# Kernel optimization log

Hardware: AMD Instinct MI355X
Metric: run time of the kernel (lower is better)

Reference implementation:

```python
import jax, jax.numpy as jnp
import numpy as np

NUM_HEADS = 6
DIM = 192
WS = (2, 6, 12)          # window size (z, h, w)
DATA = (8, 96, 180)      # padded (plev, lat, lon)
SHIFT = (1, 3, 6)


def _position_index(ws):
    Z, H, W = ws
    zi, zj = np.arange(Z), -np.arange(Z) * Z
    hi, hj = np.arange(H), -np.arange(H) * H
    w = np.arange(W)
    c1 = np.stack(np.meshgrid(zi, hi, w, indexing='ij')).reshape(3, -1)
    c2 = np.stack(np.meshgrid(zj, hj, w, indexing='ij')).reshape(3, -1)
    coords = (c1[:, :, None] - c2[:, None, :]).transpose(1, 2, 0).copy()
    coords[:, :, 2] += W - 1
    coords[:, :, 1] *= 2 * W - 1
    coords[:, :, 0] *= (2 * W - 1) * H * H
    return coords.sum(-1).reshape(-1).astype(np.int32)


def _shift_mask(data, ws, ss):
    Z, H, W = data
    img = np.zeros((Z, H, W))
    cnt = 0
    for z in ((0, -ss[0]), (-ss[0], None)):
        for h in ((0, -ss[1]), (-ss[1], None)):
            for w in ((0, None),):  # lam=False: longitude is cyclic, no w split
                img[z[0]:z[1], h[0]:h[1], w[0]:w[1]] = cnt
                cnt += 1
    m = img.reshape(Z // ws[0], ws[0], H // ws[1], ws[1], W // ws[2], ws[2])
    m = m.transpose(0, 2, 4, 1, 3, 5).reshape(-1, ws[0] * ws[1] * ws[2])
    diff = m[:, None, :] - m[:, :, None]
    return np.where(diff != 0, -100.0, 0.0).astype(np.float32)


def setup_inputs() -> dict:
    key = jax.random.key(0)
    ks = jax.random.split(key, 4)
    N = WS[0] * WS[1] * WS[2]                      # 144 tokens / window
    nW = (DATA[0] // WS[0]) * (DATA[1] // WS[1])   # 64 (z,h) window pairs
    wlon = DATA[2] // WS[2]                        # 15 lon windows
    B_ = 1 * nW * wlon                             # 960 total windows (batch=1)
    bias_rows = (2 * WS[2] - 1) * WS[1] ** 2 * WS[0] ** 2  # 3312
    return {
        'x': jax.random.normal(ks[0], (B_, N, DIM), jnp.float32),
        'w1': jax.random.normal(ks[1], (DIM, 3 * DIM), jnp.float32) * 0.02,
        'b1': jnp.zeros((3 * DIM,), jnp.float32),
        'w2': jax.random.normal(ks[2], (DIM, DIM), jnp.float32) * 0.02,
        'b2': jnp.zeros((DIM,), jnp.float32),
        'bias_table': jax.random.normal(ks[3], (bias_rows, nW, NUM_HEADS), jnp.float32) * 0.02,
        'mask': jnp.asarray(_shift_mask(DATA, WS, SHIFT)),
        'position_index': jnp.asarray(_position_index(WS)),
        'batch_size': 1,
    }


def reference(x, w1, b1, w2, b2, bias_table, mask, position_index, batch_size):
    B_, N, C = x.shape
    Ch = C // NUM_HEADS
    scale = Ch ** -0.5
    qkv = (x @ w1 + b1).reshape(B_, N, 3, NUM_HEADS, Ch)
    qkv = jnp.transpose(qkv, (2, 0, 3, 1, 4))      # (3, B_, H, N, Ch)
    q, k, v = qkv[0] * scale, qkv[1], qkv[2]
    attn = jnp.einsum('bhnc,bhmc->bhnm', q, k)      # (B_, H, N, N)
    nW = bias_table.shape[1]
    wlon = B_ // (batch_size * nW)
    # earth-specific bias gather: (N*N,) -> (nW, H, N, N)
    bias = bias_table[position_index].reshape(N, N, nW, NUM_HEADS)
    bias = jnp.transpose(bias, (2, 3, 0, 1))
    attn = attn.reshape(batch_size, nW, wlon, NUM_HEADS, N, N) + bias[None, :, None]
    # shift mask add: (total_windows, N, N) broadcast over batch and heads
    attn = attn.reshape(batch_size, nW * wlon, NUM_HEADS, N, N) + mask[None, :, None]
    attn = jax.nn.softmax(attn.reshape(B_, NUM_HEADS, N, N), axis=-1)
    out = jnp.einsum('bhnm,bhmc->bnhc', attn, v).reshape(B_, N, C)
    return out @ w2 + b2
```

## Files before the change

### kernel.cpp

```cpp
#include <hip/hip_runtime.h>

typedef __attribute__((ext_vector_type(8))) short bf16x8;
typedef __attribute__((ext_vector_type(4))) float f32x4;
typedef unsigned short u16;
typedef unsigned int u32;

#define NTOK 144
#define CDIM 192
#define NH 6
#define CH 32
#define C3 576
#define NWIN 64
#define WLON 15
#define SCALE 0.17677669529663687f
#define LOG2E 1.4426950408889634f

#define BPAD 200
#define PANEL_BYTES 25600u

#define OFF_W1T  0u
#define OFF_W2T  230400u
#define OFF_COMB 304128u
#define OFF_Q    16229376u
#define OFF_K    69313536u
#define OFF_V    122397696u

__device__ __forceinline__ u16 f2b(float f){
  u32 u = __float_as_uint(f);
  u32 r = u + 0x7FFFu + ((u >> 16) & 1u);
  return (u16)(r >> 16);
}
__device__ __forceinline__ u32 pk2(float a, float b){
  return (u32)f2b(a) | ((u32)f2b(b) << 16);
}
__device__ __forceinline__ void gload_lds16(const void* g, void* l){
  __builtin_amdgcn_global_load_lds(
      (const __attribute__((address_space(1))) unsigned int*)g,
      (__attribute__((address_space(3))) unsigned int*)l, 16, 0, 0);
}

extern "C" __global__ __launch_bounds__(256) void prep_weights(
    const float* __restrict__ w1, const float* __restrict__ w2,
    u16* __restrict__ w1tp, u16* __restrict__ w2t){
  int idx = blockIdx.x * 256 + threadIdx.x;
  if (idx < CDIM * C3){
    int k = idx / C3;  int c = idx - k * C3;
    w1tp[(size_t)c * BPAD + k] = f2b(w1[idx]);
  }
  if (idx < C3 * 8){
    int c = idx >> 3, p = idx & 7;
    w1tp[(size_t)c * BPAD + CDIM + p] = 0;
  }
  if (idx < CDIM * CDIM){ int k = idx / CDIM; int c = idx - k * CDIM; w2t[c * CDIM + k] = f2b(w2[idx]); }
}

extern "C" __global__ __launch_bounds__(192) void prep_comb(
    const float* __restrict__ bt, const float* __restrict__ mask,
    const int* __restrict__ pidx, u16* __restrict__ comb){
  int nwh = blockIdx.x;
  int nw = nwh / NH, h = nwh - nw * NH;
  int tl = blockIdx.y * 192 + threadIdx.x;
  int ti = tl / 576;
  int rem = tl - ti * 576;
  int nt = rem >> 6, lane = rem & 63;
  int ib = ti * 16 + ((lane >> 4) << 2);
  int j  = nt * 16 + (lane & 15);
  const float* mrow = mask + (size_t)(nw * WLON) * (NTOK * NTOK);
  float v[4];
  #pragma unroll
  for (int r = 0; r < 4; ++r){
    int e = (ib + r) * NTOK + j;
    int pi = pidx[e];
    v[r] = (bt[((size_t)pi * NWIN + nw) * NH + h] + mrow[e]) * LOG2E;
  }
  uint2 out; out.x = pk2(v[0], v[1]); out.y = pk2(v[2], v[3]);
  *reinterpret_cast<uint2*>(comb + ((size_t)nwh * 5184 + tl) * 4) = out;
}

extern "C" __global__ __launch_bounds__(256, 3) void qkv_gemm(
    const float* __restrict__ x, const u16* __restrict__ w1tp, const float* __restrict__ b1,
    u16* __restrict__ qw, u16* __restrict__ kw, u16* __restrict__ vw){
  __shared__ u16 Bl[2][64 * BPAD];
  const int tid = threadIdx.x;
  const int wid = tid >> 6, lane = tid & 63, l15 = lane & 15, l4 = lane >> 4;
  const size_t row0 = (size_t)blockIdx.x * 128 + wid * 32;
  const f32x4 zz = {0.f, 0.f, 0.f, 0.f};

  bf16x8 af[2][6];
  #pragma unroll
  for (int mf = 0; mf < 2; ++mf){
    const float* src = x + (row0 + mf * 16 + l15) * CDIM + l4 * 8;
    #pragma unroll
    for (int kk = 0; kk < 6; ++kk){
      float4 f0 = *reinterpret_cast<const float4*>(src + kk * 32);
      float4 f1 = *reinterpret_cast<const float4*>(src + kk * 32 + 4);
      union { bf16x8 v; uint4 u; } cv;
      cv.u.x = pk2(f0.x, f0.y); cv.u.y = pk2(f0.z, f0.w);
      cv.u.z = pk2(f1.x, f1.y); cv.u.w = pk2(f1.z, f1.w);
      af[mf][kk] = cv.v;
    }
  }
  int bw_[2], n0_[2];
  #pragma unroll
  for (int mf = 0; mf < 2; ++mf){
    int t0 = (int)row0 + mf * 16 + l4 * 4;
    bw_[mf] = t0 / NTOK; n0_[mf] = t0 - bw_[mf] * NTOK;
  }

  {
    const char* src = (const char*)w1tp + lane * 16;
    char* dst = (char*)&Bl[0][0];
    for (int j = wid; j < 25; j += 4)
      gload_lds16(src + j * 1024, dst + j * 1024);
  }

  int cur = 0;
  #pragma unroll 1
  for (int nt = 0; nt < 9; ++nt){
    __syncthreads();
    if (nt < 8){
      const char* src = (const char*)w1tp + (size_t)(nt + 1) * PANEL_BYTES + lane * 16;
      char* dst = (char*)&Bl[cur ^ 1][0];
      for (int j = wid; j < 25; j += 4)
        gload_lds16(src + j * 1024, dst + j * 1024);
    }
    f32x4 acc[2][4];
    #pragma unroll
    for (int mf = 0; mf < 2; ++mf)
      #pragma unroll
      for (int nf = 0; nf < 4; ++nf) acc[mf][nf] = zz;
    #pragma unroll
    for (int kk = 0; kk < 6; ++kk){
      bf16x8 bfr[4];
      #pragma unroll
      for (int nf = 0; nf < 4; ++nf)
        bfr[nf] = *reinterpret_cast<const bf16x8*>(&Bl[cur][(nf * 16 + l15) * BPAD + kk * 32 + l4 * 8]);
      #pragma unroll
      for (int mf = 0; mf < 2; ++mf)
        #pragma unroll
        for (int nf = 0; nf < 4; ++nf)
          acc[mf][nf] = __builtin_amdgcn_mfma_f32_16x16x32_bf16(af[mf][kk], bfr[nf], acc[mf][nf], 0, 0, 0);
    }
    int which = nt / 3;
    #pragma unroll
    for (int nf = 0; nf < 4; ++nf){
      int c = nt * 64 + nf * 16 + l15;
      int rem = c - which * CDIM;
      int hh = rem >> 5, chh = rem & 31;
      float bias = b1[c];
      if (which == 2){
        #pragma unroll
        for (int mf = 0; mf < 2; ++mf){
          uint2 pv;
          pv.x = pk2(acc[mf][nf][0] + bias, acc[mf][nf][1] + bias);
          pv.y = pk2(acc[mf][nf][2] + bias, acc[mf][nf][3] + bias);
          *reinterpret_cast<uint2*>(vw + (((size_t)bw_[mf] * NH + hh) * CH + chh) * NTOK + n0_[mf]) = pv;
        }
      } else {
        u16* base = (which == 0) ? qw : kw;
        float mult = (which == 0) ? (SCALE * LOG2E) : 1.0f;
        #pragma unroll
        for (int mf = 0; mf < 2; ++mf)
          #pragma unroll
          for (int r = 0; r < 4; ++r)
            base[(((size_t)bw_[mf] * NH + hh) * NTOK + n0_[mf] + r) * CH + chh] = f2b((acc[mf][nf][r] + bias) * mult);
      }
    }
    cur ^= 1;
  }
}

extern "C" __global__ __launch_bounds__(512) void attn_kernel(
    const u16* __restrict__ qw, const u16* __restrict__ kw, const u16* __restrict__ vw,
    const u16* __restrict__ comb, float* __restrict__ outbuf){
  __shared__ u16 Pl[8][16][40];
  const int tid = threadIdx.x;
  const int wv = tid >> 6, lane = tid & 63, l15 = lane & 15, l4 = lane >> 4;
  const int gw = blockIdx.x * 8 + wv;
  const int b = gw / NH, h = gw - b * NH;
  const size_t qkbase = ((size_t)b * NH + h) * (NTOK * CH);
  const size_t vbase  = ((size_t)b * NH + h) * (CH * NTOK);
  const u16* cb = comb + ((size_t)((b / WLON) * NH + h)) * (5184 * 4);
  u16* Pw = &Pl[wv][0][0];
  u32* stash32 = reinterpret_cast<u32*>(outbuf);
  const f32x4 zz = {0.f, 0.f, 0.f, 0.f};

  uint2 cc[9];
  #pragma unroll
  for (int nt = 0; nt < 9; ++nt)
    cc[nt] = *reinterpret_cast<const uint2*>(cb + ((size_t)nt * 64 + lane) * 4);

  #pragma unroll 1
  for (int ti = 0; ti < 9; ++ti){
    const int tin = (ti < 8) ? ti + 1 : ti;
    uint2 ccn[9];
    #pragma unroll
    for (int nt = 0; nt < 9; ++nt)
      ccn[nt] = *reinterpret_cast<const uint2*>(cb + ((size_t)(tin * 9 + nt) * 64 + lane) * 4);

    bf16x8 aq = *reinterpret_cast<const bf16x8*>(qw + qkbase + (ti * 16 + l15) * CH + l4 * 8);
    f32x4 s[9];
    #pragma unroll
    for (int nt = 0; nt < 9; ++nt){
      f32x4 cf;
      cf[0] = __uint_as_float(cc[nt].x << 16);
      cf[1] = __uint_as_float(cc[nt].x & 0xFFFF0000u);
      cf[2] = __uint_as_float(cc[nt].y << 16);
      cf[3] = __uint_as_float(cc[nt].y & 0xFFFF0000u);
      bf16x8 bk = *reinterpret_cast<const bf16x8*>(kw + qkbase + (nt * 16 + l15) * CH + l4 * 8);
      s[nt] = __builtin_amdgcn_mfma_f32_16x16x32_bf16(aq, bk, cf, 0, 0, 0);
    }
    float invs[4];
    #pragma unroll
    for (int r = 0; r < 4; ++r){
      float sum = 0.f;
      #pragma unroll
      for (int nt = 0; nt < 9; ++nt){
        float p = exp2f(s[nt][r]);
        s[nt][r] = p; sum += p;
      }
      #pragma unroll
      for (int off = 8; off; off >>= 1) sum += __shfl_xor(sum, off, 16);
      invs[r] = 1.0f / sum;
    }
    f32x4 oe = zz, oo = zz;
    #pragma unroll
    for (int kk = 0; kk < 5; ++kk){
      #pragma unroll
      for (int r = 0; r < 4; ++r){
        Pw[(l4 * 4 + r) * 40 + l15] = f2b(s[2 * kk][r]);
        if (kk < 4) Pw[(l4 * 4 + r) * 40 + 16 + l15] = f2b(s[2 * kk + 1][r]);
      }
      int j0 = kk * 32 + l4 * 8;
      int jc = (j0 < NTOK) ? j0 : 0;
      bf16x8 ap = *reinterpret_cast<const bf16x8*>(Pw + l15 * 40 + l4 * 8);
      bf16x8 bve = *reinterpret_cast<const bf16x8*>(vw + vbase + (size_t)(2 * l15) * NTOK + jc);
      bf16x8 bvo = *reinterpret_cast<const bf16x8*>(vw + vbase + (size_t)(2 * l15 + 1) * NTOK + jc);
      if (j0 >= NTOK) ap = bf16x8{0, 0, 0, 0, 0, 0, 0, 0};
      oe = __builtin_amdgcn_mfma_f32_16x16x32_bf16(ap, bve, oe, 0, 0, 0);
      oo = __builtin_amdgcn_mfma_f32_16x16x32_bf16(ap, bvo, oo, 0, 0, 0);
    }
    #pragma unroll
    for (int r = 0; r < 4; ++r){
      size_t t = (size_t)b * NTOK + ti * 16 + l4 * 4 + r;
      float is = invs[r];
      stash32[t * 192 + 96 + h * 16 + l15] = pk2(oe[r] * is, oo[r] * is);
    }
    #pragma unroll
    for (int nt = 0; nt < 9; ++nt) cc[nt] = ccn[nt];
  }
}

extern "C" __global__ __launch_bounds__(256, 2) void proj_gemm(
    const u16* __restrict__ w2t, const float* __restrict__ b2, float* __restrict__ outbuf){
  const int tid = threadIdx.x;
  const int wid = tid >> 6, lane = tid & 63, l15 = lane & 15, l4 = lane >> 4;
  const int hb = blockIdx.y;
  const f32x4 zz = {0.f, 0.f, 0.f, 0.f};

  bf16x8 bfr[6][6];
  #pragma unroll
  for (int nf = 0; nf < 6; ++nf)
    #pragma unroll
    for (int kk = 0; kk < 6; ++kk)
      bfr[nf][kk] = *reinterpret_cast<const bf16x8*>(
          w2t + (size_t)(hb * 96 + nf * 16 + l15) * CDIM + kk * 32 + l4 * 8);

  const u16* stash = reinterpret_cast<const u16*>(outbuf);
  const size_t rbase = (size_t)blockIdx.x * 256 + wid * 64;

#define LOADA(dst, mt) { \
    const u16* src_ = stash + (rbase + (mt) * 16 + l15) * 384 + 192 + l4 * 8; \
    _Pragma("unroll") \
    for (int kk = 0; kk < 6; ++kk) dst[kk] = *reinterpret_cast<const bf16x8*>(src_ + kk * 32); }

#define COMPUTE(a_, mt) { \
    f32x4 acc[6]; \
    _Pragma("unroll") \
    for (int nf = 0; nf < 6; ++nf) acc[nf] = zz; \
    _Pragma("unroll") \
    for (int kk = 0; kk < 6; ++kk) \
      _Pragma("unroll") \
      for (int nf = 0; nf < 6; ++nf) \
        acc[nf] = __builtin_amdgcn_mfma_f32_16x16x32_bf16(a_[kk], bfr[nf][kk], acc[nf], 0, 0, 0); \
    _Pragma("unroll") \
    for (int nf = 0; nf < 6; ++nf){ \
      int c = hb * 96 + nf * 16 + l15; \
      float bias = b2[c]; \
      _Pragma("unroll") \
      for (int r = 0; r < 4; ++r) \
        outbuf[(rbase + (mt) * 16 + l4 * 4 + r) * CDIM + c] = acc[nf][r] + bias; } }

  bf16x8 a0[6], a1[6];
  LOADA(a0, 0)
  LOADA(a1, 1) COMPUTE(a0, 0)
  LOADA(a0, 2) COMPUTE(a1, 1)
  LOADA(a1, 3) COMPUTE(a0, 2)
  COMPUTE(a1, 3)
#undef LOADA
#undef COMPUTE
}

extern "C" void kernel_launch(void* const* d_in, const int* in_sizes, int n_in,
                              void* d_out, int out_size, void* d_ws, size_t ws_size,
                              hipStream_t stream){
  const float* x    = (const float*)d_in[0];
  const float* w1   = (const float*)d_in[1];
  const float* b1   = (const float*)d_in[2];
  const float* w2   = (const float*)d_in[3];
  const float* b2   = (const float*)d_in[4];
  const float* bt   = (const float*)d_in[5];
  const float* mask = (const float*)d_in[6];
  const int*   pidx = (const int*)d_in[7];
  (void)in_sizes; (void)n_in; (void)out_size; (void)ws_size;

  char* ws = (char*)d_ws;
  u16*   w1tp = (u16*)(ws + OFF_W1T);
  u16*   w2t  = (u16*)(ws + OFF_W2T);
  u16*   comb = (u16*)(ws + OFF_COMB);
  u16*   qw   = (u16*)(ws + OFF_Q);
  u16*   kw   = (u16*)(ws + OFF_K);
  u16*   vw   = (u16*)(ws + OFF_V);
  float* out = (float*)d_out;

  prep_weights<<<dim3(432), dim3(256), 0, stream>>>(w1, w2, w1tp, w2t);
  prep_comb<<<dim3(384, 27), dim3(192), 0, stream>>>(bt, mask, pidx, comb);
  qkv_gemm<<<dim3(1080), dim3(256), 0, stream>>>(x, w1tp, b1, qw, kw, vw);
  attn_kernel<<<dim3(720), dim3(512), 0, stream>>>(qw, kw, vw, comb, out);
  proj_gemm<<<dim3(540, 2), dim3(256), 0, stream>>>(w2t, b2, out);
}
```

Before: 245.3 us.

## Fuse output projection into attention kernel via per-window LDS staging

Each block now handles one window, with six waves covering the six heads. Attention outputs are written into an LDS tile instead of being stashed as bf16 in the output buffer. After a block barrier, each wave computes 32 output columns of the projection GEMM from LDS and writes the final fp32 result. This removes the proj_gemm launch and the global round trip of the intermediate, at the cost of a larger LDS footprint (~58KB), which may reduce occupancy, and a 384-thread block shape.

Result: slower. 251.7 us (+2.6%).

```diff
diff --git a/kernel.cpp b/kernel.cpp
--- a/kernel.cpp
+++ b/kernel.cpp
@@ -170,19 +170,21 @@
   }
 }
 
-extern "C" __global__ __launch_bounds__(512) void attn_kernel(
+extern "C" __global__ __launch_bounds__(384) void attn_proj(
     const u16* __restrict__ qw, const u16* __restrict__ kw, const u16* __restrict__ vw,
-    const u16* __restrict__ comb, float* __restrict__ outbuf){
-  __shared__ u16 Pl[8][16][40];
+    const u16* __restrict__ comb, const u16* __restrict__ w2t, const float* __restrict__ b2,
+    float* __restrict__ outbuf){
+  __shared__ u16 Olds[NTOK * 200];
+  __shared__ u16 Pl[6][16][40];
   const int tid = threadIdx.x;
-  const int wv = tid >> 6, lane = tid & 63, l15 = lane & 15, l4 = lane >> 4;
-  const int gw = blockIdx.x * 8 + wv;
-  const int b = gw / NH, h = gw - b * NH;
+  const int b = blockIdx.x;
+  const int h = tid >> 6;
+  const int lane = tid & 63, l15 = lane & 15, l4 = lane >> 4;
   const size_t qkbase = ((size_t)b * NH + h) * (NTOK * CH);
   const size_t vbase  = ((size_t)b * NH + h) * (CH * NTOK);
   const u16* cb = comb + ((size_t)((b / WLON) * NH + h)) * (5184 * 4);
-  u16* Pw = &Pl[wv][0][0];
-  u32* stash32 = reinterpret_cast<u32*>(outbuf);
+  u16* Pw = &Pl[h][0][0];
+  u32* O32 = reinterpret_cast<u32*>(Olds);
   const f32x4 zz = {0.f, 0.f, 0.f, 0.f};
 
   uint2 cc[9];
@@ -242,63 +244,48 @@
     }
     #pragma unroll
     for (int r = 0; r < 4; ++r){
-      size_t t = (size_t)b * NTOK + ti * 16 + l4 * 4 + r;
+      int t = ti * 16 + l4 * 4 + r;
       float is = invs[r];
-      stash32[t * 192 + 96 + h * 16 + l15] = pk2(oe[r] * is, oo[r] * is);
+      O32[t * 100 + h * 16 + l15] = pk2(oe[r] * is, oo[r] * is);
     }
     #pragma unroll
     for (int nt = 0; nt < 9; ++nt) cc[nt] = ccn[nt];
   }
-}
-
-extern "C" __global__ __launch_bounds__(256, 2) void proj_gemm(
-    const u16* __restrict__ w2t, const float* __restrict__ b2, float* __restrict__ outbuf){
-  const int tid = threadIdx.x;
-  const int wid = tid >> 6, lane = tid & 63, l15 = lane & 15, l4 = lane >> 4;
-  const int hb = blockIdx.y;
-  const f32x4 zz = {0.f, 0.f, 0.f, 0.f};
-
-  bf16x8 bfr[6][6];
-  #pragma unroll
-  for (int nf = 0; nf < 6; ++nf)
+
+  bf16x8 bfr[2][6];
+  #pragma unroll
+  for (int nf = 0; nf < 2; ++nf)
     #pragma unroll
     for (int kk = 0; kk < 6; ++kk)
       bfr[nf][kk] = *reinterpret_cast<const bf16x8*>(
-          w2t + (size_t)(hb * 96 + nf * 16 + l15) * CDIM + kk * 32 + l4 * 8);
-
-  const u16* stash = reinterpret_cast<const u16*>(outbuf);
-  const size_t rbase = (size_t)blockIdx.x * 256 + wid * 64;
-
-#define LOADA(dst, mt) { \
-    const u16* src_ = stash + (rbase + (mt) * 16 + l15) * 384 + 192 + l4 * 8; \
-    _Pragma("unroll") \
-    for (int kk = 0; kk < 6; ++kk) dst[kk] = *reinterpret_cast<const bf16x8*>(src_ + kk * 32); }
-
-#define COMPUTE(a_, mt) { \
-    f32x4 acc[6]; \
-    _Pragma("unroll") \
-    for (int nf = 0; nf < 6; ++nf) acc[nf] = zz; \
-    _Pragma("unroll") \
-    for (int kk = 0; kk < 6; ++kk) \
-      _Pragma("unroll") \
-      for (int nf = 0; nf < 6; ++nf) \
-        acc[nf] = __builtin_amdgcn_mfma_f32_16x16x32_bf16(a_[kk], bfr[nf][kk], acc[nf], 0, 0, 0); \
-    _Pragma("unroll") \
-    for (int nf = 0; nf < 6; ++nf){ \
-      int c = hb * 96 + nf * 16 + l15; \
-      float bias = b2[c]; \
-      _Pragma("unroll") \
-      for (int r = 0; r < 4; ++r) \
-        outbuf[(rbase + (mt) * 16 + l4 * 4 + r) * CDIM + c] = acc[nf][r] + bias; } }
-
-  bf16x8 a0[6], a1[6];
-  LOADA(a0, 0)
-  LOADA(a1, 1) COMPUTE(a0, 0)
-  LOADA(a0, 2) COMPUTE(a1, 1)
-  LOADA(a1, 3) COMPUTE(a0, 2)
-  COMPUTE(a1, 3)
-#undef LOADA
-#undef COMPUTE
+          w2t + (size_t)(h * 32 + nf * 16 + l15) * CDIM + kk * 32 + l4 * 8);
+  float bias[2];
+  #pragma unroll
+  for (int nf = 0; nf < 2; ++nf) bias[nf] = b2[h * 32 + nf * 16 + l15];
+
+  __syncthreads();
+
+  #pragma unroll 1
+  for (int mt = 0; mt < 9; ++mt){
+    bf16x8 afr[6];
+    #pragma unroll
+    for (int kk = 0; kk < 6; ++kk)
+      afr[kk] = *reinterpret_cast<const bf16x8*>(Olds + (mt * 16 + l15) * 200 + kk * 32 + l4 * 8);
+    f32x4 acc[2];
+    acc[0] = zz; acc[1] = zz;
+    #pragma unroll
+    for (int kk = 0; kk < 6; ++kk){
+      acc[0] = __builtin_amdgcn_mfma_f32_16x16x32_bf16(afr[kk], bfr[0][kk], acc[0], 0, 0, 0);
+      acc[1] = __builtin_amdgcn_mfma_f32_16x16x32_bf16(afr[kk], bfr[1][kk], acc[1], 0, 0, 0);
+    }
+    #pragma unroll
+    for (int nf = 0; nf < 2; ++nf){
+      int c = h * 32 + nf * 16 + l15;
+      #pragma unroll
+      for (int r = 0; r < 4; ++r)
+        outbuf[((size_t)b * NTOK + mt * 16 + l4 * 4 + r) * CDIM + c] = acc[nf][r] + bias[nf];
+    }
+  }
 }
 
 extern "C" void kernel_launch(void* const* d_in, const int* in_sizes, int n_in,
@@ -326,6 +313,5 @@
   prep_weights<<<dim3(432), dim3(256), 0, stream>>>(w1, w2, w1tp, w2t);
   prep_comb<<<dim3(384, 27), dim3(192), 0, stream>>>(bt, mask, pidx, comb);
   qkv_gemm<<<dim3(1080), dim3(256), 0, stream>>>(x, w1tp, b1, qw, kw, vw);
-  attn_kernel<<<dim3(720), dim3(512), 0, stream>>>(qw, kw, vw, comb, out);
-  proj_gemm<<<dim3(540, 2), dim3(256), 0, stream>>>(w2t, b2, out);
-}
+  attn_proj<<<dim3(960), dim3(384), 0, stream>>>(qw, kw, vw, comb, w2t, b2, out);
+}
```
